# Optimization experiments

Hardware: AMD Instinct MI355X
Metric: run time of the kernel (lower is better)

## Reference

```python
import jax, jax.numpy as jnp
import numpy as np

B, C, H, W = 4, 192, 128, 128
NH = 6
HD = C // NH            # 32
GS = 8                  # window (group) size
K = 16                  # unfold kernel size
STRIDE, PAD = 8, 4
NUM = H // GS           # 16 groups per side
BG = B * NUM * NUM      # 1024 windows
N = GS * GS             # 64 tokens per group
KK = K * K              # 256 sampled tokens per window
SCALE = HD ** -0.5


def _rope(x):
    # lucidrains-style rotary embedding along dim -2 (positions), last dim = head_dim
    d = x.shape[-1]
    inv = 1.0 / (10000.0 ** (jnp.arange(0, d, 2, dtype=jnp.float32) / d))
    t = jnp.arange(x.shape[-2], dtype=jnp.float32)
    freqs = jnp.repeat(t[:, None] * inv[None, :], 2, axis=-1)  # [seq, d], interleaved
    cos, sin = jnp.cos(freqs), jnp.sin(freqs)
    xp = x.reshape(x.shape[:-1] + (d // 2, 2))
    xr = jnp.stack((-xp[..., 1], xp[..., 0]), axis=-1).reshape(x.shape)
    return x * cos + xr * sin


def _l2norm(x):
    # torch F.normalize(dim=-1): x / max(||x||, eps)
    n = jnp.linalg.norm(x, axis=-1, keepdims=True)
    return x / jnp.maximum(n, 1e-12)


def setup_inputs() -> dict:
    key = jax.random.key(0)
    ks = jax.random.split(key, 6)
    return {
        "x_complete": jax.random.normal(ks[0], (B, C, H, W), jnp.float32),
        "graph": jax.random.randint(ks[1], (BG, 1, N, KK), 0, 2) > 0,
        "w_group": jax.random.normal(ks[2], (C, C), jnp.float32) * 0.02,
        "b_group": jnp.zeros((C,), jnp.float32),
        "w_sample": jax.random.normal(ks[3], (2 * C, C), jnp.float32) * 0.02,
        "b_sample": jnp.zeros((2 * C,), jnp.float32),
        "w_proj": jax.random.normal(ks[4], (C, C), jnp.float32) * 0.02,
        "b_proj": jnp.zeros((C,), jnp.float32),
    }


def reference(x_complete, graph, w_group, b_group, w_sample, b_sample, w_proj, b_proj):
    # --- local grouping: [B,C,(numh sh),(numw sw)] -> [(B numh numw), sh*sw, C]
    xg = x_complete.reshape(B, C, NUM, GS, NUM, GS).transpose(0, 2, 4, 3, 5, 1).reshape(BG, N, C)
    # --- proj_group: 1x1 Conv1d over channels, then split heads 'b (h c) n -> b h n c'
    x1 = jnp.einsum('bnc,dc->bnd', xg, w_group) + b_group
    x1 = x1.reshape(BG, N, NH, HD).transpose(0, 2, 1, 3)            # [BG,NH,N,HD]
    # --- proj_sample: 1x1 Conv2d to 2C channels
    xs = jnp.einsum('bchw,dc->bdhw', x_complete, w_sample) + b_sample[None, :, None, None]
    # --- F.unfold(kernel=16, stride=8, pad=4): patch features channel-major (c,k0,k1)
    patches = jax.lax.conv_general_dilated_patches(
        xs, (K, K), (STRIDE, STRIDE), ((PAD, PAD), (PAD, PAD)))    # [B, 2C*KK, NUM, NUM]
    xs = patches.reshape(B, 2 * C, KK, NUM * NUM).transpose(0, 3, 2, 1).reshape(BG, KK, 2 * C)
    # --- 'b n (div h c) -> div b h n c'
    xs = xs.reshape(BG, KK, 2, NH, HD)
    x2 = xs[:, :, 0].transpose(0, 2, 1, 3)                          # [BG,NH,KK,HD]
    feat = xs[:, :, 1].transpose(0, 2, 1, 3)                        # [BG,NH,KK,HD]
    # --- RoPE + masked cosine-sim attention
    q = _rope(x1)
    k = _rope(x2)
    sim = jnp.einsum('bhmc,bhnc->bhmn', _l2norm(q), _l2norm(k))
    sim = sim + (-100.0) * (~graph).astype(sim.dtype)
    corr = jax.nn.softmax(sim * SCALE, axis=-1)                     # [BG,NH,N,KK]
    out = jnp.einsum('bhmn,bhnc->bhmc', corr, feat)                 # [BG,NH,N,HD]
    out = out.transpose(0, 2, 1, 3).reshape(BG, N, C)
    return out @ w_proj.T + b_proj
```

## Files before the change

### kernel.cpp

```cpp
#include <hip/hip_runtime.h>
#include <hip/hip_bf16.h>

#define B_    4
#define C_    192
#define C2_   384
#define PIX_  16384
#define NH_   6
#define BG_   1024
#define SCALE_ 0.17677669529663687f
#define NEGM_ (-17.677669529663685f)

typedef __attribute__((ext_vector_type(8))) short short8v;
typedef __attribute__((ext_vector_type(4))) float f32x4;

__global__ __launch_bounds__(256, 1)
void k_rope_init(float2* __restrict__ tbl) {
    int e = blockIdx.x * 256 + threadIdx.x;
    if (e >= 4096) return;
    int pos = e >> 4, j = e & 15;
    float freq = powf(10.0f, -0.25f * (float)j);
    float ang = (float)pos * freq;
    float sn, cs;
    sincosf(ang, &sn, &cs);
    tbl[e] = make_float2(cs, sn);
}

__global__ __launch_bounds__(256, 4)
void k_gmask(const int* __restrict__ g, unsigned int* __restrict__ gbits) {
    int e = blockIdx.x * 256 + threadIdx.x;
    const uint4* p = (const uint4*)(g + (size_t)e * 32);
    unsigned int m = 0u;
#pragma unroll
    for (int i = 0; i < 8; ++i) {
        uint4 v = p[i];
        m |= (v.x ? 1u : 0u) << (i * 4);
        m |= (v.y ? 1u : 0u) << (i * 4 + 1);
        m |= (v.z ? 1u : 0u) << (i * 4 + 2);
        m |= (v.w ? 1u : 0u) << (i * 4 + 3);
    }
    gbits[e] = m;
}

__global__ __launch_bounds__(256, 4)
void k_wcast(const float* __restrict__ wsm, const float* __restrict__ wgb,
             const float* __restrict__ wpj, __hip_bfloat16* __restrict__ wb)
{
    int e = (blockIdx.x * 256 + threadIdx.x) * 4;
    float4 v = (e < 73728) ? *(const float4*)(wsm + e)
             : (e < 110592) ? *(const float4*)(wgb + (e - 73728))
                            : *(const float4*)(wpj + (e - 110592));
    union { uint2 u; __hip_bfloat16 h[4]; } pk;
    pk.h[0] = __float2bfloat16(v.x); pk.h[1] = __float2bfloat16(v.y);
    pk.h[2] = __float2bfloat16(v.z); pk.h[3] = __float2bfloat16(v.w);
    *(uint2*)(wb + e) = pk.u;
}

__global__ __launch_bounds__(256, 4)
void k_convm(const float* __restrict__ x, const __hip_bfloat16* __restrict__ wb,
             const float* __restrict__ bsm, const float* __restrict__ bgb,
             const float2* __restrict__ tbl,
             __hip_bfloat16* __restrict__ xsk, __hip_bfloat16* __restrict__ xsv,
             __hip_bfloat16* __restrict__ qbf)
{
    __shared__ __align__(16) char smem[25600];
    const int bid0 = blockIdx.x;
    const int bid = (bid0 & 7) * 1152 + (bid0 >> 3);
    const int oct = bid % 9;
    const int pb  = bid / 9;
    const int b = pb >> 8, pt = pb & 255;
    const int px0 = pt * 64;
    const int t = threadIdx.x;

    {
        const int px = t & 63, cq = t >> 6;
        const float* src = x + ((size_t)b * C_ + cq * 48) * PIX_ + px0 + px;
        char* row = smem + px * 400 + cq * 96;
#pragma unroll
        for (int i = 0; i < 6; ++i) {
            union { uint4 u; __hip_bfloat16 h[8]; } pk;
#pragma unroll
            for (int j = 0; j < 8; ++j)
                pk.h[j] = __float2bfloat16(src[(size_t)(i * 8 + j) * PIX_]);
            *(uint4*)(row + i * 16) = pk.u;
        }
    }
    __syncthreads();

    const int w = t >> 6, lane = t & 63;
    const int l15 = lane & 15, g = lane >> 4;
    const int mb = (w & 1) * 32;
    const int nb = (w >> 1) * 32;

    const f32x4 zz = {0.0f, 0.0f, 0.0f, 0.0f};
    f32x4 acc00 = zz, acc01 = zz, acc10 = zz, acc11 = zz;
    const __hip_bfloat16* w0 = wb + (size_t)(oct * 64 + nb + l15) * C_;
    const __hip_bfloat16* w1 = w0 + 16 * C_;
#pragma unroll
    for (int ks = 0; ks < 6; ++ks) {
        const short8v a0 = *(const short8v*)(smem + (mb + l15) * 400      + ks * 64 + g * 16);
        const short8v a1 = *(const short8v*)(smem + (mb + 16 + l15) * 400 + ks * 64 + g * 16);
        const short8v b0 = *(const short8v*)(w0 + ks * 32 + g * 8);
        const short8v b1 = *(const short8v*)(w1 + ks * 32 + g * 8);
        acc00 = __builtin_amdgcn_mfma_f32_16x16x32_bf16(a0, b0, acc00, 0, 0, 0);
        acc01 = __builtin_amdgcn_mfma_f32_16x16x32_bf16(a0, b1, acc01, 0, 0, 0);
        acc10 = __builtin_amdgcn_mfma_f32_16x16x32_bf16(a1, b0, acc10, 0, 0, 0);
        acc11 = __builtin_amdgcn_mfma_f32_16x16x32_bf16(a1, b1, acc11, 0, 0, 0);
    }
    __syncthreads();

    float* ot = (float*)smem;
    if (oct >= 3 && oct < 6) {
        *(f32x4*)&ot[(nb + l15) * 68      + mb + g * 4]      = acc00;
        *(f32x4*)&ot[(nb + l15) * 68      + mb + 16 + g * 4] = acc10;
        *(f32x4*)&ot[(nb + 16 + l15) * 68 + mb + g * 4]      = acc01;
        *(f32x4*)&ot[(nb + 16 + l15) * 68 + mb + 16 + g * 4] = acc11;
        __syncthreads();
        const float* bias = bsm + oct * 64;
#pragma unroll
        for (int e0 = 0; e0 < 2; ++e0) {
            const int e = e0 * 256 + t;
            const int oc = e >> 3, seg = e & 7;
            const float bo = bias[oc];
            float4 v0 = *(const float4*)&ot[oc * 68 + seg * 8];
            float4 v1 = *(const float4*)&ot[oc * 68 + seg * 8 + 4];
            union { uint4 u; __hip_bfloat16 h[8]; } pk;
            pk.h[0] = __float2bfloat16(v0.x + bo); pk.h[1] = __float2bfloat16(v0.y + bo);
            pk.h[2] = __float2bfloat16(v0.z + bo); pk.h[3] = __float2bfloat16(v0.w + bo);
            pk.h[4] = __float2bfloat16(v1.x + bo); pk.h[5] = __float2bfloat16(v1.y + bo);
            pk.h[6] = __float2bfloat16(v1.z + bo); pk.h[7] = __float2bfloat16(v1.w + bo);
            *(uint4*)(xsv + (size_t)(b * C_ + (oct - 3) * 64 + oc) * PIX_ + px0 + seg * 8) = pk.u;
        }
    } else {
#pragma unroll
        for (int j = 0; j < 4; ++j) {
            ot[(mb + g * 4 + j) * 68      + nb + l15]      = acc00[j];
            ot[(mb + 16 + g * 4 + j) * 68 + nb + l15]      = acc10[j];
            ot[(mb + g * 4 + j) * 68      + nb + 16 + l15] = acc01[j];
            ot[(mb + 16 + g * 4 + j) * 68 + nb + 16 + l15] = acc11[j];
        }
        __syncthreads();
        if (oct < 3) {
            const int px = t >> 2, i = t & 3;
            const int ocb = oct * 64 + i * 16;
            union { uint4 u[2]; __hip_bfloat16 h[16]; } pk;
#pragma unroll
            for (int q4 = 0; q4 < 4; ++q4) {
                float4 v  = *(const float4*)&ot[px * 68 + i * 16 + q4 * 4];
                float4 bv = *(const float4*)(bsm + ocb + q4 * 4);
                pk.h[q4 * 4 + 0] = __float2bfloat16(v.x + bv.x);
                pk.h[q4 * 4 + 1] = __float2bfloat16(v.y + bv.y);
                pk.h[q4 * 4 + 2] = __float2bfloat16(v.z + bv.z);
                pk.h[q4 * 4 + 3] = __float2bfloat16(v.w + bv.w);
            }
            __hip_bfloat16* dst = xsk + ((size_t)b * PIX_ + px0 + px) * C_ + ocb;
            *(uint4*)dst       = pk.u[0];
            *(uint4*)(dst + 8) = pk.u[1];
        } else {
            const int px = t & 63, hh = t >> 6;
            if (hh < 2) {
                const int p = px0 + px;
                const int r = p >> 7, c = p & 127;
                const int n = (r & 7) * 8 + (c & 7);
                const int bg = (b << 8) + ((r >> 3) << 4) + (c >> 3);
                const int hglob = (oct - 6) * 2 + hh;
                float v[32];
#pragma unroll
                for (int d4 = 0; d4 < 8; ++d4) {
                    float4 vv = *(const float4*)&ot[px * 68 + hh * 32 + d4 * 4];
                    float4 bv = *(const float4*)(bgb + hglob * 32 + d4 * 4);
                    v[d4 * 4 + 0] = vv.x + bv.x; v[d4 * 4 + 1] = vv.y + bv.y;
                    v[d4 * 4 + 2] = vv.z + bv.z; v[d4 * 4 + 3] = vv.w + bv.w;
                }
                float rr[32];
#pragma unroll
                for (int j = 0; j < 16; ++j) {
                    float2 cs = tbl[n * 16 + j];
                    float a0 = v[2 * j], a1 = v[2 * j + 1];
                    rr[2 * j]     = a0 * cs.x - a1 * cs.y;
                    rr[2 * j + 1] = a1 * cs.x + a0 * cs.y;
                }
                float n2 = 0.0f;
#pragma unroll
                for (int d = 0; d < 32; ++d) n2 = fmaf(rr[d], rr[d], n2);
                const float inv = 1.0f / fmaxf(sqrtf(n2), 1e-12f);
                __hip_bfloat16* dst = qbf + ((size_t)(bg * NH_ + hglob) * 64 + n) * 32;
#pragma unroll
                for (int c8 = 0; c8 < 4; ++c8) {
                    union { uint4 u; __hip_bfloat16 h[8]; } pk;
#pragma unroll
                    for (int i = 0; i < 8; ++i) pk.h[i] = __float2bfloat16(rr[c8 * 8 + i] * inv);
                    *(uint4*)(dst + c8 * 8) = pk.u;
                }
            }
        }
    }
}

__global__ __launch_bounds__(512, 2)
void k_attn(const __hip_bfloat16* __restrict__ xsk, const __hip_bfloat16* __restrict__ xsv,
            const unsigned int* __restrict__ gbits, const __hip_bfloat16* __restrict__ qb,
            const float2* __restrict__ tbl, float* __restrict__ attn)
{
    __shared__ __align__(16) char smem[52736];
    const int bid0 = blockIdx.x;
    const int bid = (bid0 & 7) * 768 + (bid0 >> 3);
    const int h = bid % NH_;
    const int bg = bid / NH_;
    const int b = bg >> 8, ph = (bg >> 4) & 15, pw = bg & 15;
    const int t = threadIdx.x;
    const int w = t >> 6, lane = t & 63;
    const int g = lane >> 4, l15 = lane & 15;
    const int rbase = (w & 3) * 16;
    const int wcol  = w >> 2;
    const int cb    = wcol * 128;
    const int cb32  = wcol * 4;

    const short8v qa = *(const short8v*)(qb +
        ((size_t)(bg * NH_ + h) * 64 + rbase + l15) * 32 + g * 8);

    {
        const int m = t >> 1, half = t & 1;
        const int k0 = m >> 4, k1 = m & 15;
        const int rr = ph * 8 - 4 + k0, cc = pw * 8 - 4 + k1;
        const bool inb = ((unsigned)rr < 128u) && ((unsigned)cc < 128u);
        float kv[16];
        if (inb) {
            const uint4* pk = (const uint4*)(xsk +
                ((size_t)b * PIX_ + rr * 128 + cc) * C_ + h * 32 + half * 16);
            union { uint4 u; __hip_bfloat16 h8[8]; } r0, r1;
            r0.u = pk[0]; r1.u = pk[1];
#pragma unroll
            for (int d = 0; d < 8; ++d) {
                kv[d]     = __bfloat162float(r0.h8[d]);
                kv[8 + d] = __bfloat162float(r1.h8[d]);
            }
        } else {
#pragma unroll
            for (int d = 0; d < 16; ++d) kv[d] = 0.0f;
        }
#pragma unroll
        for (int p = 0; p < 8; ++p) {
            float2 cs = tbl[m * 16 + half * 8 + p];
            float a0 = kv[2 * p], a1 = kv[2 * p + 1];
            kv[2 * p]     = a0 * cs.x - a1 * cs.y;
            kv[2 * p + 1] = a1 * cs.x + a0 * cs.y;
        }
        float n2 = 0.0f;
#pragma unroll
        for (int d = 0; d < 16; ++d) n2 = fmaf(kv[d], kv[d], n2);
        n2 += __shfl_xor(n2, 1);
        const float inv = 1.0f / fmaxf(sqrtf(n2), 1e-12f);
        union { uint4 u; __hip_bfloat16 hh[8]; } p0, p1;
#pragma unroll
        for (int i = 0; i < 8; ++i) {
            p0.hh[i] = __float2bfloat16(kv[i] * inv);
            p1.hh[i] = __float2bfloat16(kv[8 + i] * inv);
        }
        *(uint4*)(smem + m * 80 + half * 32)      = p0.u;
        *(uint4*)(smem + m * 80 + half * 32 + 16) = p1.u;
    }

    {
        const int d = t & 31, k0 = t >> 5;
        const int rr = ph * 8 - 4 + k0;
        const int c0 = pw * 8 - 4;
        char* dst = smem + 34816 + d * 528 + k0 * 32;
        const __hip_bfloat16* src = xsv + (size_t)(b * C_ + h * 32 + d) * PIX_ + rr * 128 + c0;
        const bool rok = (unsigned)rr < 128u;
        if (rok && pw >= 1 && pw <= 14) {
            const uint2* s2 = (const uint2*)src;
            uint2 a0 = s2[0], a1 = s2[1], a2 = s2[2], a3 = s2[3];
            ((uint4*)dst)[0] = make_uint4(a0.x, a0.y, a1.x, a1.y);
            ((uint4*)dst)[1] = make_uint4(a2.x, a2.y, a3.x, a3.y);
        } else {
            __hip_bfloat16* dh = (__hip_bfloat16*)dst;
            __hip_bfloat16 z = __float2bfloat16(0.0f);
#pragma unroll
            for (int i = 0; i < 16; ++i) {
                bool ok = rok && ((unsigned)(c0 + i) < 128u);
                dh[i] = ok ? src[i] : z;
            }
        }
    }

    {
        unsigned int* gbl = (unsigned int*)(smem + 20480);
        const int q = t >> 3, wd = t & 7;
        gbl[q * 9 + wd] = gbits[(size_t)bg * 512 + t];
    }
    __syncthreads();

    f32x4 acc[8];
    const f32x4 zz = {0.0f, 0.0f, 0.0f, 0.0f};
#pragma unroll
    for (int tile = 0; tile < 8; ++tile) {
        const short8v kb = *(const short8v*)(smem + (cb + tile * 16 + l15) * 80 + g * 16);
        acc[tile] = __builtin_amdgcn_mfma_f32_16x16x32_bf16(qa, kb, zz, 0, 0, 0);
    }

    const unsigned int* gbl = (const unsigned int*)(smem + 20480);
    float* redm = (float*)(smem + 51712);
    float* reds = (float*)(smem + 51712 + 512);
    float mx4[4], Mt[4], sm4[4], inv4[4];
#pragma unroll
    for (int j = 0; j < 4; ++j) {
        const int q = rbase + g * 4 + j;
        const unsigned int wv[4] = { gbl[q * 9 + cb32], gbl[q * 9 + cb32 + 1],
                                     gbl[q * 9 + cb32 + 2], gbl[q * 9 + cb32 + 3] };
        float mx = -3.0e38f;
#pragma unroll
        for (int tile = 0; tile < 8; ++tile) {
            unsigned int bit = (wv[tile >> 1] >> ((tile & 1) * 16 + l15)) & 1u;
            float s = acc[tile][j] * SCALE_ + (bit ? 0.0f : NEGM_);
            acc[tile][j] = s;
            mx = fmaxf(mx, s);
        }
        mx = fmaxf(mx, __shfl_xor(mx, 1));
        mx = fmaxf(mx, __shfl_xor(mx, 2));
        mx = fmaxf(mx, __shfl_xor(mx, 4));
        mx = fmaxf(mx, __shfl_xor(mx, 8));
        mx4[j] = mx;
        if (l15 == 0) redm[wcol * 64 + q] = mx;
    }
    __syncthreads();
#pragma unroll
    for (int j = 0; j < 4; ++j) {
        const int q = rbase + g * 4 + j;
        Mt[j] = fmaxf(mx4[j], redm[(wcol ^ 1) * 64 + q]);
        float sm = 0.0f;
#pragma unroll
        for (int tile = 0; tile < 8; ++tile) {
            float e = __expf(acc[tile][j] - Mt[j]);
            acc[tile][j] = e;
            sm += e;
        }
        sm += __shfl_xor(sm, 1);
        sm += __shfl_xor(sm, 2);
        sm += __shfl_xor(sm, 4);
        sm += __shfl_xor(sm, 8);
        sm4[j] = sm;
        if (l15 == 0) reds[wcol * 64 + q] = sm;
    }
    __syncthreads();
#pragma unroll
    for (int j = 0; j < 4; ++j) {
        const int q = rbase + g * 4 + j;
        inv4[j] = 1.0f / (sm4[j] + reds[(wcol ^ 1) * 64 + q]);
    }

    char* plw = smem + w * 4352;
#pragma unroll
    for (int tile = 0; tile < 8; ++tile)
#pragma unroll
        for (int j = 0; j < 4; ++j) {
            *(__hip_bfloat16*)(plw + (g * 4 + j) * 272 + (tile * 16 + l15) * 2) =
                __float2bfloat16(acc[tile][j] * inv4[j]);
        }

    f32x4 o0 = zz, o1 = zz;
#pragma unroll
    for (int ks = 0; ks < 4; ++ks) {
        const short8v pa  = *(const short8v*)(plw + l15 * 272 + (ks * 32 + g * 8) * 2);
        const short8v vb0 = *(const short8v*)(smem + 34816 + l15 * 528        + (cb + ks * 32 + g * 8) * 2);
        const short8v vb1 = *(const short8v*)(smem + 34816 + (16 + l15) * 528 + (cb + ks * 32 + g * 8) * 2);
        o0 = __builtin_amdgcn_mfma_f32_16x16x32_bf16(pa, vb0, o0, 0, 0, 0);
        o1 = __builtin_amdgcn_mfma_f32_16x16x32_bf16(pa, vb1, o1, 0, 0, 0);
    }
    __syncthreads();

    float* ob = (float*)smem;
    if (wcol == 1) {
#pragma unroll
        for (int j = 0; j < 4; ++j) {
            const int q = rbase + g * 4 + j;
            ob[q * 33 + l15]      = o0[j];
            ob[q * 33 + 16 + l15] = o1[j];
        }
    }
    __syncthreads();
    if (wcol == 0) {
#pragma unroll
        for (int j = 0; j < 4; ++j) {
            const int q = rbase + g * 4 + j;
            float v0 = o0[j] + ob[q * 33 + l15];
            float v1 = o1[j] + ob[q * 33 + 16 + l15];
            attn[((size_t)bg * 64 + q) * 192 + h * 32 + l15]      = v0;
            attn[((size_t)bg * 64 + q) * 192 + h * 32 + 16 + l15] = v1;
        }
    }
}

__global__ __launch_bounds__(256, 4)
void k_oprojm(const float* __restrict__ attn, const __hip_bfloat16* __restrict__ wpb,
              const float* __restrict__ bp, float* __restrict__ out)
{
    __shared__ __align__(16) char smem[25600];
    const int bid0 = blockIdx.x;
    const int bid = (bid0 & 7) * 384 + (bid0 >> 3);
    const int oct = bid % 3;
    const int rt  = bid / 3;
    const int row0 = rt * 64;
    const int t = threadIdx.x;

#pragma unroll
    for (int e0 = 0; e0 < 12; ++e0) {
        const int e = e0 * 256 + t;
        const int r = e / 48, c4 = e % 48;
        float4 v = *(const float4*)(attn + (size_t)(row0 + r) * 192 + c4 * 4);
        union { uint2 u; __hip_bfloat16 h[4]; } pk;
        pk.h[0] = __float2bfloat16(v.x); pk.h[1] = __float2bfloat16(v.y);
        pk.h[2] = __float2bfloat16(v.z); pk.h[3] = __float2bfloat16(v.w);
        *(uint2*)(smem + r * 400 + c4 * 8) = pk.u;
    }
    __syncthreads();

    const int w = t >> 6, lane = t & 63;
    const int l15 = lane & 15, g = lane >> 4;
    const int mb = (w & 1) * 32;
    const int nb = (w >> 1) * 32;

    const f32x4 zz = {0.0f, 0.0f, 0.0f, 0.0f};
    f32x4 acc00 = zz, acc01 = zz, acc10 = zz, acc11 = zz;
    const __hip_bfloat16* w0 = wpb + (size_t)(oct * 64 + nb + l15) * C_;
    const __hip_bfloat16* w1 = w0 + 16 * C_;
#pragma unroll
    for (int ks = 0; ks < 6; ++ks) {
        const short8v a0 = *(const short8v*)(smem + (mb + l15) * 400      + ks * 64 + g * 16);
        const short8v a1 = *(const short8v*)(smem + (mb + 16 + l15) * 400 + ks * 64 + g * 16);
        const short8v b0 = *(const short8v*)(w0 + ks * 32 + g * 8);
        const short8v b1 = *(const short8v*)(w1 + ks * 32 + g * 8);
        acc00 = __builtin_amdgcn_mfma_f32_16x16x32_bf16(a0, b0, acc00, 0, 0, 0);
        acc01 = __builtin_amdgcn_mfma_f32_16x16x32_bf16(a0, b1, acc01, 0, 0, 0);
        acc10 = __builtin_amdgcn_mfma_f32_16x16x32_bf16(a1, b0, acc10, 0, 0, 0);
        acc11 = __builtin_amdgcn_mfma_f32_16x16x32_bf16(a1, b1, acc11, 0, 0, 0);
    }
    __syncthreads();

    float* ot = (float*)smem;
#pragma unroll
    for (int j = 0; j < 4; ++j) {
        ot[(mb + g * 4 + j) * 68      + nb + l15]      = acc00[j];
        ot[(mb + 16 + g * 4 + j) * 68 + nb + l15]      = acc10[j];
        ot[(mb + g * 4 + j) * 68      + nb + 16 + l15] = acc01[j];
        ot[(mb + 16 + g * 4 + j) * 68 + nb + 16 + l15] = acc11[j];
    }
    __syncthreads();

    {
        const int k = t & 15, pxi = t >> 4;
        const float4 bias4 = *(const float4*)(bp + oct * 64 + k * 4);
#pragma unroll
        for (int p = 0; p < 4; ++p) {
            const int px = p * 16 + pxi;
            float4 v = *(const float4*)&ot[px * 68 + k * 4];
            v.x += bias4.x; v.y += bias4.y; v.z += bias4.z; v.w += bias4.w;
            *(float4*)(out + (size_t)(row0 + px) * 192 + oct * 64 + k * 4) = v;
        }
    }
}

extern "C" void kernel_launch(void* const* d_in, const int* in_sizes, int n_in,
                              void* d_out, int out_size, void* d_ws, size_t ws_size,
                              hipStream_t stream)
{
    (void)in_sizes; (void)n_in; (void)out_size; (void)ws_size;
    const float* x   = (const float*)d_in[0];
    const int* grph  = (const int*)d_in[1];
    const float* wg  = (const float*)d_in[2];
    const float* bgb = (const float*)d_in[3];
    const float* wsm = (const float*)d_in[4];
    const float* bsm = (const float*)d_in[5];
    const float* wp  = (const float*)d_in[6];
    const float* bp  = (const float*)d_in[7];
    float* out = (float*)d_out;

    char* wsb = (char*)d_ws;
    __hip_bfloat16* xsk = (__hip_bfloat16*)wsb;
    __hip_bfloat16* xsv = (__hip_bfloat16*)(wsb + 25165824ull);
    __hip_bfloat16* qbf = (__hip_bfloat16*)(wsb + 50331648ull);
    float2* tbl = (float2*)(wsb + 75497472ull);
    unsigned int* gbits = (unsigned int*)(wsb + 75530240ull);
    __hip_bfloat16* wb  = (__hip_bfloat16*)(wsb + 77627392ull);
    __hip_bfloat16* wpb = wb + 110592;

    hipLaunchKernelGGL(k_rope_init, dim3(16),   dim3(256), 0, stream, tbl);
    hipLaunchKernelGGL(k_wcast,     dim3(144),  dim3(256), 0, stream, wsm, wg, wp, wb);
    hipLaunchKernelGGL(k_gmask,     dim3(2048), dim3(256), 0, stream, grph, gbits);
    hipLaunchKernelGGL(k_convm,     dim3(9216), dim3(256), 0, stream, x, wb, bsm, bgb, tbl, xsk, xsv, qbf);
    hipLaunchKernelGGL(k_attn,      dim3(6144), dim3(512), 0, stream, xsk, xsv, gbits, qbf, tbl, out);
    hipLaunchKernelGGL(k_oprojm,    dim3(3072), dim3(256), 0, stream, out, wpb, bp, out);
}
```

Baseline: 215.5 us.

## Compute all nine output slices per conv block and pre-normalize keys in conv

Each k_convm block now converts its 64-pixel input tile to bf16 once, keeps the A fragments in registers, and loops over all nine 64-channel output slices. Before, nine separate blocks each reloaded and reconverted the same fp32 input. The grid shrinks from 9216 to 1024 blocks. The per-head L2 normalization of the key features also moves from the attention kernel into the conv epilogue. This relies on RoPE being a rotation that preserves the norm. It trades fewer redundant global reads and less attention-side work for lower block-level parallelism, more serialized work per block, and higher register pressure.

New measurement: 207.9 us. 1.04x faster.

```diff
diff --git a/kernel.cpp b/kernel.cpp
--- a/kernel.cpp
+++ b/kernel.cpp
@@ -63,11 +63,8 @@
              __hip_bfloat16* __restrict__ qbf)
 {
     __shared__ __align__(16) char smem[25600];
-    const int bid0 = blockIdx.x;
-    const int bid = (bid0 & 7) * 1152 + (bid0 >> 3);
-    const int oct = bid % 9;
-    const int pb  = bid / 9;
-    const int b = pb >> 8, pt = pb & 255;
+    const int bid = blockIdx.x;
+    const int b = bid >> 8, pt = bid & 255;
     const int px0 = pt * 64;
     const int t = threadIdx.x;
 
@@ -91,70 +88,86 @@
     const int mb = (w & 1) * 32;
     const int nb = (w >> 1) * 32;
 
+    short8v a0r[6], a1r[6];
+#pragma unroll
+    for (int ks = 0; ks < 6; ++ks) {
+        a0r[ks] = *(const short8v*)(smem + (mb + l15) * 400      + ks * 64 + g * 16);
+        a1r[ks] = *(const short8v*)(smem + (mb + 16 + l15) * 400 + ks * 64 + g * 16);
+    }
+    __syncthreads();
+
+    float* ot = (float*)smem;
     const f32x4 zz = {0.0f, 0.0f, 0.0f, 0.0f};
-    f32x4 acc00 = zz, acc01 = zz, acc10 = zz, acc11 = zz;
-    const __hip_bfloat16* w0 = wb + (size_t)(oct * 64 + nb + l15) * C_;
-    const __hip_bfloat16* w1 = w0 + 16 * C_;
-#pragma unroll
-    for (int ks = 0; ks < 6; ++ks) {
-        const short8v a0 = *(const short8v*)(smem + (mb + l15) * 400      + ks * 64 + g * 16);
-        const short8v a1 = *(const short8v*)(smem + (mb + 16 + l15) * 400 + ks * 64 + g * 16);
-        const short8v b0 = *(const short8v*)(w0 + ks * 32 + g * 8);
-        const short8v b1 = *(const short8v*)(w1 + ks * 32 + g * 8);
-        acc00 = __builtin_amdgcn_mfma_f32_16x16x32_bf16(a0, b0, acc00, 0, 0, 0);
-        acc01 = __builtin_amdgcn_mfma_f32_16x16x32_bf16(a0, b1, acc01, 0, 0, 0);
-        acc10 = __builtin_amdgcn_mfma_f32_16x16x32_bf16(a1, b0, acc10, 0, 0, 0);
-        acc11 = __builtin_amdgcn_mfma_f32_16x16x32_bf16(a1, b1, acc11, 0, 0, 0);
-    }
-    __syncthreads();
-
-    float* ot = (float*)smem;
-    if (oct >= 3 && oct < 6) {
-        *(f32x4*)&ot[(nb + l15) * 68      + mb + g * 4]      = acc00;
-        *(f32x4*)&ot[(nb + l15) * 68      + mb + 16 + g * 4] = acc10;
-        *(f32x4*)&ot[(nb + 16 + l15) * 68 + mb + g * 4]      = acc01;
-        *(f32x4*)&ot[(nb + 16 + l15) * 68 + mb + 16 + g * 4] = acc11;
+
+    for (int oct = 0; oct < 9; ++oct) {
+        f32x4 acc00 = zz, acc01 = zz, acc10 = zz, acc11 = zz;
+        const __hip_bfloat16* w0 = wb + (size_t)(oct * 64 + nb + l15) * C_;
+        const __hip_bfloat16* w1 = w0 + 16 * C_;
+#pragma unroll
+        for (int ks = 0; ks < 6; ++ks) {
+            const short8v b0 = *(const short8v*)(w0 + ks * 32 + g * 8);
+            const short8v b1 = *(const short8v*)(w1 + ks * 32 + g * 8);
+            acc00 = __builtin_amdgcn_mfma_f32_16x16x32_bf16(a0r[ks], b0, acc00, 0, 0, 0);
+            acc01 = __builtin_amdgcn_mfma_f32_16x16x32_bf16(a0r[ks], b1, acc01, 0, 0, 0);
+            acc10 = __builtin_amdgcn_mfma_f32_16x16x32_bf16(a1r[ks], b0, acc10, 0, 0, 0);
+            acc11 = __builtin_amdgcn_mfma_f32_16x16x32_bf16(a1r[ks], b1, acc11, 0, 0, 0);
+        }
         __syncthreads();
-        const float* bias = bsm + oct * 64;
-#pragma unroll
-        for (int e0 = 0; e0 < 2; ++e0) {
-            const int e = e0 * 256 + t;
-            const int oc = e >> 3, seg = e & 7;
-            const float bo = bias[oc];
-            float4 v0 = *(const float4*)&ot[oc * 68 + seg * 8];
-            float4 v1 = *(const float4*)&ot[oc * 68 + seg * 8 + 4];
-            union { uint4 u; __hip_bfloat16 h[8]; } pk;
-            pk.h[0] = __float2bfloat16(v0.x + bo); pk.h[1] = __float2bfloat16(v0.y + bo);
-            pk.h[2] = __float2bfloat16(v0.z + bo); pk.h[3] = __float2bfloat16(v0.w + bo);
-            pk.h[4] = __float2bfloat16(v1.x + bo); pk.h[5] = __float2bfloat16(v1.y + bo);
-            pk.h[6] = __float2bfloat16(v1.z + bo); pk.h[7] = __float2bfloat16(v1.w + bo);
-            *(uint4*)(xsv + (size_t)(b * C_ + (oct - 3) * 64 + oc) * PIX_ + px0 + seg * 8) = pk.u;
-        }
-    } else {
-#pragma unroll
-        for (int j = 0; j < 4; ++j) {
-            ot[(mb + g * 4 + j) * 68      + nb + l15]      = acc00[j];
-            ot[(mb + 16 + g * 4 + j) * 68 + nb + l15]      = acc10[j];
-            ot[(mb + g * 4 + j) * 68      + nb + 16 + l15] = acc01[j];
-            ot[(mb + 16 + g * 4 + j) * 68 + nb + 16 + l15] = acc11[j];
+
+        if (oct >= 3 && oct < 6) {
+            *(f32x4*)&ot[(nb + l15) * 68      + mb + g * 4]      = acc00;
+            *(f32x4*)&ot[(nb + l15) * 68      + mb + 16 + g * 4] = acc10;
+            *(f32x4*)&ot[(nb + 16 + l15) * 68 + mb + g * 4]      = acc01;
+            *(f32x4*)&ot[(nb + 16 + l15) * 68 + mb + 16 + g * 4] = acc11;
+        } else {
+#pragma unroll
+            for (int j = 0; j < 4; ++j) {
+                ot[(mb + g * 4 + j) * 68      + nb + l15]      = acc00[j];
+                ot[(mb + 16 + g * 4 + j) * 68 + nb + l15]      = acc10[j];
+                ot[(mb + g * 4 + j) * 68      + nb + 16 + l15] = acc01[j];
+                ot[(mb + 16 + g * 4 + j) * 68 + nb + 16 + l15] = acc11[j];
+            }
         }
         __syncthreads();
+
         if (oct < 3) {
             const int px = t >> 2, i = t & 3;
             const int ocb = oct * 64 + i * 16;
+            float v[16];
+#pragma unroll
+            for (int q4 = 0; q4 < 4; ++q4) {
+                float4 vv = *(const float4*)&ot[px * 68 + i * 16 + q4 * 4];
+                float4 bv = *(const float4*)(bsm + ocb + q4 * 4);
+                v[q4 * 4 + 0] = vv.x + bv.x; v[q4 * 4 + 1] = vv.y + bv.y;
+                v[q4 * 4 + 2] = vv.z + bv.z; v[q4 * 4 + 3] = vv.w + bv.w;
+            }
+            float n2 = 0.0f;
+#pragma unroll
+            for (int d = 0; d < 16; ++d) n2 = fmaf(v[d], v[d], n2);
+            n2 += __shfl_xor(n2, 1);
+            const float inv = 1.0f / fmaxf(sqrtf(n2), 1e-12f);
             union { uint4 u[2]; __hip_bfloat16 h[16]; } pk;
 #pragma unroll
-            for (int q4 = 0; q4 < 4; ++q4) {
-                float4 v  = *(const float4*)&ot[px * 68 + i * 16 + q4 * 4];
-                float4 bv = *(const float4*)(bsm + ocb + q4 * 4);
-                pk.h[q4 * 4 + 0] = __float2bfloat16(v.x + bv.x);
-                pk.h[q4 * 4 + 1] = __float2bfloat16(v.y + bv.y);
-                pk.h[q4 * 4 + 2] = __float2bfloat16(v.z + bv.z);
-                pk.h[q4 * 4 + 3] = __float2bfloat16(v.w + bv.w);
-            }
+            for (int d = 0; d < 16; ++d) pk.h[d] = __float2bfloat16(v[d] * inv);
             __hip_bfloat16* dst = xsk + ((size_t)b * PIX_ + px0 + px) * C_ + ocb;
             *(uint4*)dst       = pk.u[0];
             *(uint4*)(dst + 8) = pk.u[1];
+        } else if (oct < 6) {
+            const float* bias = bsm + oct * 64;
+#pragma unroll
+            for (int e0 = 0; e0 < 2; ++e0) {
+                const int e = e0 * 256 + t;
+                const int oc = e >> 3, seg = e & 7;
+                const float bo = bias[oc];
+                float4 v0 = *(const float4*)&ot[oc * 68 + seg * 8];
+                float4 v1 = *(const float4*)&ot[oc * 68 + seg * 8 + 4];
+                union { uint4 u; __hip_bfloat16 h[8]; } pk;
+                pk.h[0] = __float2bfloat16(v0.x + bo); pk.h[1] = __float2bfloat16(v0.y + bo);
+                pk.h[2] = __float2bfloat16(v0.z + bo); pk.h[3] = __float2bfloat16(v0.w + bo);
+                pk.h[4] = __float2bfloat16(v1.x + bo); pk.h[5] = __float2bfloat16(v1.y + bo);
+                pk.h[6] = __float2bfloat16(v1.z + bo); pk.h[7] = __float2bfloat16(v1.w + bo);
+                *(uint4*)(xsv + (size_t)(b * C_ + (oct - 3) * 64 + oc) * PIX_ + px0 + seg * 8) = pk.u;
+            }
         } else {
             const int px = t & 63, hh = t >> 6;
             if (hh < 2) {
@@ -238,23 +251,15 @@
 #pragma unroll
             for (int d = 0; d < 16; ++d) kv[d] = 0.0f;
         }
+        union { uint4 u; __hip_bfloat16 hh[8]; } p0, p1;
 #pragma unroll
         for (int p = 0; p < 8; ++p) {
             float2 cs = tbl[m * 16 + half * 8 + p];
             float a0 = kv[2 * p], a1 = kv[2 * p + 1];
-            kv[2 * p]     = a0 * cs.x - a1 * cs.y;
-            kv[2 * p + 1] = a1 * cs.x + a0 * cs.y;
-        }
-        float n2 = 0.0f;
-#pragma unroll
-        for (int d = 0; d < 16; ++d) n2 = fmaf(kv[d], kv[d], n2);
-        n2 += __shfl_xor(n2, 1);
-        const float inv = 1.0f / fmaxf(sqrtf(n2), 1e-12f);
-        union { uint4 u; __hip_bfloat16 hh[8]; } p0, p1;
-#pragma unroll
-        for (int i = 0; i < 8; ++i) {
-            p0.hh[i] = __float2bfloat16(kv[i] * inv);
-            p1.hh[i] = __float2bfloat16(kv[8 + i] * inv);
+            float e0 = a0 * cs.x - a1 * cs.y;
+            float e1 = a1 * cs.x + a0 * cs.y;
+            if (p < 4) { p0.hh[2 * p] = __float2bfloat16(e0); p0.hh[2 * p + 1] = __float2bfloat16(e1); }
+            else { p1.hh[2 * (p - 4)] = __float2bfloat16(e0); p1.hh[2 * (p - 4) + 1] = __float2bfloat16(e1); }
         }
         *(uint4*)(smem + m * 80 + half * 32)      = p0.u;
         *(uint4*)(smem + m * 80 + half * 32 + 16) = p1.u;
@@ -486,7 +491,7 @@
     hipLaunchKernelGGL(k_rope_init, dim3(16),   dim3(256), 0, stream, tbl);
     hipLaunchKernelGGL(k_wcast,     dim3(144),  dim3(256), 0, stream, wsm, wg, wp, wb);
     hipLaunchKernelGGL(k_gmask,     dim3(2048), dim3(256), 0, stream, grph, gbits);
-    hipLaunchKernelGGL(k_convm,     dim3(9216), dim3(256), 0, stream, x, wb, bsm, bgb, tbl, xsk, xsv, qbf);
+    hipLaunchKernelGGL(k_convm,     dim3(1024), dim3(256), 0, stream, x, wb, bsm, bgb, tbl, xsk, xsv, qbf);
     hipLaunchKernelGGL(k_attn,      dim3(6144), dim3(512), 0, stream, xsk, xsv, gbits, qbf, tbl, out);
     hipLaunchKernelGGL(k_oprojm,    dim3(3072), dim3(256), 0, stream, out, wpb, bp, out);
 }
```
